# Kernel optimization log

Hardware: AMD Instinct MI355X
Metric: run time of the kernel (lower is better)

The kernel has to match this reference:

```python
import jax, jax.numpy as jnp
import numpy as np

B, L, C, DK, M, R = 8, 2048, 512, 64, 8, 64
H = 2 * C  # GLU hidden size
NEG = -32767.0  # -2**15 + 1 masked_fill value


def _ln(x, g, b):
    m = x.mean(-1, keepdims=True)
    v = jnp.mean((x - m) ** 2, axis=-1, keepdims=True)
    return (x - m) * jax.lax.rsqrt(v + 1e-5) * g + b


def setup_inputs() -> dict:
    key = jax.random.key(0)
    ks = jax.random.split(key, 16)
    p = lambda k, sh: 0.02 * jax.random.normal(k, sh, dtype=jnp.float32)
    return {
        "qx": jax.random.normal(ks[0], (B, L, C), dtype=jnp.float32),
        "vx": jax.random.normal(ks[1], (B, L, C), dtype=jnp.float32),
        "maskPAD2": jax.random.randint(ks[2], (B, 1, L), 0, 2),
        "WQ1": p(ks[3], (C, M * DK)), "WK1": p(ks[4], (C, M * DK)),
        "WV1": p(ks[5], (C, M * DK)), "WO1": p(ks[6], (M * DK, C)),
        "qln_g": jnp.ones((C,), jnp.float32), "qln_b": jnp.zeros((C,), jnp.float32),
        "Wp": p(ks[7], (C, R)), "bp": jnp.zeros((R,), jnp.float32),
        "Wq2": p(ks[8], (C, DK)), "bq2": jnp.zeros((DK,), jnp.float32),
        "Wk2": p(ks[9], (C, DK)), "bk2": jnp.zeros((DK,), jnp.float32),
        "Wv2": p(ks[10], (C, H)), "bv2": jnp.zeros((H,), jnp.float32),
        "Wu": p(ks[11], (C, H)), "bu": jnp.zeros((H,), jnp.float32),
        "Wo2": p(ks[12], (H, C)), "bo2": jnp.zeros((C,), jnp.float32),
        "ln_g": jnp.ones((C,), jnp.float32), "ln_b": jnp.zeros((C,), jnp.float32),
    }


def _forward(qx, vx, maskPAD2, WQ1, WK1, WV1, WO1, qln_g, qln_b,
             Wp, bp, Wq2, bq2, Wk2, bk2, Wv2, bv2, Wu, bu, Wo2, bo2, ln_g, ln_b):
    b, ql, c = qx.shape
    # ---- SelfAttention_CumNext(qx, qx, qx) ----
    div = jnp.arange(1, ql + 1, dtype=qx.dtype)[None, :, None]
    vc = jnp.cumsum(qx, axis=1) / div                      # running mean, [B,L,C]
    q = (qx @ WQ1).reshape(b, ql, M, DK).transpose(0, 2, 1, 3)   # [B,M,L,dk]
    k = (vc @ WK1).reshape(b, ql, M, DK).transpose(0, 2, 1, 3)
    v = (vc @ WV1).reshape(b, ql, M, DK).transpose(0, 2, 1, 3)
    scores1 = jnp.sum(q[:, :, 1:] * k[:, :, :-1], axis=-1, keepdims=True) / np.sqrt(DK)
    z = jax.nn.sigmoid(scores1) * v[:, :, :-1]             # [B,M,L-1,dk]
    z = z.transpose(0, 2, 1, 3).reshape(b, ql - 1, M * DK) @ WO1
    z = jnp.pad(z, ((0, 0), (1, 0), (0, 0)))               # shift right by 1
    qx = _ln(qx + z, qln_g, qln_b)
    # ---- GLU gate ----
    gate = jax.nn.silu(qx @ Wu + bu)                       # [B,L,2C]
    # ---- Linformer-style pseudo attention over vx ----
    pScore = vx @ Wp + bp                                  # [B,kvL,r]
    mask = (maskPAD2[:, 0] == 0)[..., None]                # [B,kvL,1]
    pScore = jnp.where(mask, NEG, pScore)
    pAlpha = jax.nn.softmax(pScore, axis=1)                # softmax over kvL
    pkvx = jnp.einsum('blr,blc->brc', pAlpha, vx)          # [B,r,C]
    queries = jax.nn.silu(qx @ Wq2 + bq2)                  # [B,L,dk]
    keys = jax.nn.silu(pkvx @ Wk2 + bk2)                   # [B,r,dk]
    values = jax.nn.silu(pkvx @ Wv2 + bv2)                 # [B,r,2C]
    scores2 = jnp.einsum('bld,brd->blr', queries, keys) / np.sqrt(DK)
    alpha = jax.nn.softmax(scores2, axis=-1)
    z2 = jnp.einsum('blr,brh->blh', alpha, values)         # [B,L,2C]
    z2 = (gate * z2) @ Wo2 + bo2                           # [B,L,C]
    return _ln(qx + z2, ln_g, ln_b)


def reference(qx, vx, maskPAD2, WQ1, WK1, WV1, WO1, qln_g, qln_b,
              Wp, bp, Wq2, bq2, Wk2, bk2, Wv2, bv2, Wu, bu, Wo2, bo2, ln_g, ln_b):
    return _forward(qx, vx, maskPAD2, WQ1, WK1, WV1, WO1, qln_g, qln_b,
                    Wp, bp, Wq2, bq2, Wk2, bk2, Wv2, bv2, Wu, bu, Wo2, bo2, ln_g, ln_b)
```

## Files before the change

kernel.cpp:

```cpp
#include <hip/hip_runtime.h>
#include <hip/hip_bf16.h>

#define B_ 8
#define L_ 2048
#define C_ 512
#define DK_ 64
#define M_ 8
#define R_ 64
#define H_ 1024
#define N_ (B_*L_)
#define NEG_ (-32767.0f)
#define NSEG 32
#define SEGLEN 64

typedef short bf16x8 __attribute__((ext_vector_type(8)));
typedef unsigned short us8 __attribute__((ext_vector_type(8)));
typedef float f32x4v __attribute__((ext_vector_type(4)));

__device__ __forceinline__ float siluf_(float x) { return x / (1.0f + expf(-x)); }

__device__ __forceinline__ unsigned short f2bf(float f) {
    __hip_bfloat16 h = __float2bfloat16(f);
    return __builtin_bit_cast(unsigned short, h);
}
__device__ __forceinline__ float bf2f(unsigned short u) {
    unsigned v = (unsigned)u << 16;
    return __builtin_bit_cast(float, v);
}

__device__ __forceinline__ void gload_lds16(const void* g, void* l) {
    __builtin_amdgcn_global_load_lds(
        (const __attribute__((address_space(1))) unsigned int*)(uintptr_t)g,
        (__attribute__((address_space(3))) unsigned int*)(unsigned)(uintptr_t)l,
        16, 0, 0);
}

__global__ __launch_bounds__(256) void cvt2_kernel(const float* __restrict__ s0,
                                                   const float* __restrict__ s1,
                                                   unsigned short* __restrict__ d0,
                                                   unsigned short* __restrict__ d1) {
    const float* s = blockIdx.z ? s1 : s0;
    unsigned short* d = blockIdx.z ? d1 : d0;
    const size_t i = ((size_t)blockIdx.x * 256 + threadIdx.x) * 8;
    const float4 v0 = *(const float4*)(s + i);
    const float4 v1 = *(const float4*)(s + i + 4);
    us8 o;
    o[0] = f2bf(v0.x); o[1] = f2bf(v0.y); o[2] = f2bf(v0.z); o[3] = f2bf(v0.w);
    o[4] = f2bf(v1.x); o[5] = f2bf(v1.y); o[6] = f2bf(v1.z); o[7] = f2bf(v1.w);
    *(us8*)(d + i) = o;
}

struct WtDesc { const float* src; unsigned short* dst; int K; int N; };
struct WtArgs { WtDesc d[10]; };

__global__ __launch_bounds__(256) void wtrans_all_kernel(WtArgs a) {
    const WtDesc w = a.d[blockIdx.z];
    const int n0 = blockIdx.x * 32, k0 = blockIdx.y * 32;
    if (n0 >= w.N || k0 >= w.K) return;
    __shared__ float t[32][33];
    const int tx = threadIdx.x, ty = threadIdx.y;
    #pragma unroll
    for (int i = 0; i < 32; i += 8)
        t[ty + i][tx] = w.src[(size_t)(k0 + ty + i) * w.N + n0 + tx];
    __syncthreads();
    #pragma unroll
    for (int i = 0; i < 32; i += 8)
        w.dst[(size_t)(n0 + ty + i) * w.K + k0 + tx] = f2bf(t[tx][ty + i]);
}

__global__ __launch_bounds__(512) void seg_sum_kernel(const unsigned short* __restrict__ qx,
                                                      float* __restrict__ segsum) {
    const int seg = blockIdx.x, b = blockIdx.y, c = threadIdx.x;
    const unsigned short* p = qx + ((size_t)b * L_ + (size_t)seg * SEGLEN) * C_ + c;
    float s = 0.f;
    #pragma unroll 8
    for (int i = 0; i < SEGLEN; ++i) s += bf2f(p[(size_t)i * C_]);
    segsum[((size_t)b * NSEG + seg) * C_ + c] = s;
}

__global__ __launch_bounds__(512) void seg_scan_kernel(const unsigned short* __restrict__ qx,
                                                       const float* __restrict__ segsum,
                                                       unsigned short* __restrict__ vc) {
    const int seg = blockIdx.x, b = blockIdx.y, c = threadIdx.x;
    float off = 0.f;
    for (int s = 0; s < seg; ++s) off += segsum[((size_t)b * NSEG + s) * C_ + c];
    const unsigned short* p = qx + ((size_t)b * L_ + (size_t)seg * SEGLEN) * C_ + c;
    unsigned short* o = vc + ((size_t)b * L_ + (size_t)seg * SEGLEN) * C_ + c;
    float run = off;
    for (int i = 0; i < SEGLEN; ++i) {
        run += bf2f(p[(size_t)i * C_]);
        const int l = seg * SEGLEN + i;
        o[(size_t)i * C_] = f2bf(run / (float)(l + 1));
    }
}

template<int BN, int ACT, bool BIAS, int OUT>
__global__ __launch_bounds__(256) void gemm_bf16(const unsigned short* __restrict__ A,
                                                 const unsigned short* __restrict__ Wt,
                                                 const float* __restrict__ bias,
                                                 void* __restrict__ Cout,
                                                 int K, int N) {
    constexpr int BK = 64;
    constexpr int WN = BN / 2;
    constexpr int TN = WN / 16;
    __shared__ unsigned short Alds[128 * BK];
    __shared__ unsigned short Blds[BN * BK];
    const int tid = threadIdx.x;
    const int w = tid >> 6, lane = tid & 63;
    const int wm = w >> 1, wn = w & 1;
    const int m0 = blockIdx.x * 128, n0 = blockIdx.y * BN;

    f32x4v acc[4][TN];
    #pragma unroll
    for (int m = 0; m < 4; ++m)
        #pragma unroll
        for (int n = 0; n < TN; ++n)
            acc[m][n] = f32x4v{0.f, 0.f, 0.f, 0.f};

    const int lrow = lane >> 3;
    const int lk = (lane & 7) * 8;

    for (int k0 = 0; k0 < K; k0 += BK) {
        __syncthreads();
        #pragma unroll
        for (int i = 0; i < 4; ++i) {
            const int c = w * 4 + i;
            const int row = c * 8 + lrow;
            gload_lds16(A + (size_t)(m0 + row) * K + k0 + lk, (char*)Alds + c * 1024);
        }
        #pragma unroll
        for (int i = 0; i < BN / 32; ++i) {
            const int c = w * (BN / 32) + i;
            const int col = c * 8 + lrow;
            gload_lds16(Wt + (size_t)(n0 + col) * K + k0 + lk, (char*)Blds + c * 1024);
        }
        __syncthreads();
        #pragma unroll
        for (int kk = 0; kk < 2; ++kk) {
            const int ko = kk * 64 + (lane >> 4) * 16;
            bf16x8 af[4], bfr[TN];
            #pragma unroll
            for (int m = 0; m < 4; ++m)
                af[m] = *(const bf16x8*)((const char*)Alds + (wm * 64 + m * 16 + (lane & 15)) * 128 + ko);
            #pragma unroll
            for (int n = 0; n < TN; ++n)
                bfr[n] = *(const bf16x8*)((const char*)Blds + (wn * WN + n * 16 + (lane & 15)) * 128 + ko);
            #pragma unroll
            for (int m = 0; m < 4; ++m)
                #pragma unroll
                for (int n = 0; n < TN; ++n)
                    acc[m][n] = __builtin_amdgcn_mfma_f32_16x16x32_bf16(af[m], bfr[n], acc[m][n], 0, 0, 0);
        }
    }
    const int r0 = (lane >> 4) * 4;
    #pragma unroll
    for (int n = 0; n < TN; ++n) {
        const int gc = n0 + wn * WN + n * 16 + (lane & 15);
        float bv = 0.f;
        if constexpr (BIAS) bv = bias[gc];
        #pragma unroll
        for (int m = 0; m < 4; ++m) {
            const int gr = m0 + wm * 64 + m * 16 + r0;
            float val[4];
            #pragma unroll
            for (int r = 0; r < 4; ++r) {
                val[r] = acc[m][n][r] + bv;
                if constexpr (ACT == 1) val[r] = siluf_(val[r]);
            }
            if constexpr (OUT == 0) {
                #pragma unroll
                for (int r = 0; r < 4; ++r)
                    ((float*)Cout)[(size_t)(gr + r) * N + gc] = val[r];
            } else if constexpr (OUT == 1) {
                #pragma unroll
                for (int r = 0; r < 4; ++r)
                    ((unsigned short*)Cout)[(size_t)(gr + r) * N + gc] = f2bf(val[r]);
            } else {
                ushort4 pk;
                pk.x = f2bf(val[0]); pk.y = f2bf(val[1]);
                pk.z = f2bf(val[2]); pk.w = f2bf(val[3]);
                *(ushort4*)((unsigned short*)Cout + ((size_t)(gr >> 6) * N + gc) * 64 + (gr & 63)) = pk;
            }
        }
    }
}

__global__ __launch_bounds__(512) void attn1_kernel(const unsigned short* __restrict__ Q,
                                                    const unsigned short* __restrict__ KV,
                                                    unsigned short* __restrict__ zbf) {
    const int l = blockIdx.x, b = blockIdx.y;
    const size_t row = ((size_t)b * L_ + l) * 512;
    if (l == 0) { zbf[row + threadIdx.x] = 0; return; }
    const size_t rowp = ((size_t)b * L_ + l - 1) * 1024;
    const float qv = bf2f(Q[row + threadIdx.x]);
    const float kv = bf2f(KV[rowp + threadIdx.x]);
    float p = qv * kv;
    #pragma unroll
    for (int o = 32; o; o >>= 1) p += __shfl_xor(p, o);
    const float s = p * 0.125f;
    const float sig = 1.0f / (1.0f + expf(-s));
    const float vv = bf2f(KV[rowp + 512 + threadIdx.x]);
    zbf[row + threadIdx.x] = f2bf(sig * vv);
}

__global__ __launch_bounds__(256) void ln_kernel(const float* __restrict__ X,
                                                 const float* __restrict__ Y,
                                                 const float* __restrict__ g,
                                                 const float* __restrict__ beta,
                                                 float* __restrict__ out,
                                                 unsigned short* __restrict__ outb) {
    const int w = threadIdx.x >> 6, lane = threadIdx.x & 63;
    const size_t row = (size_t)blockIdx.x * 4 + w;
    const float4* x4 = (const float4*)(X + row * C_);
    const float4* y4 = (const float4*)(Y + row * C_);
    float v[8];
    const float4 a = x4[lane * 2 + 0], b2 = x4[lane * 2 + 1];
    const float4 c = y4[lane * 2 + 0], d = y4[lane * 2 + 1];
    v[0] = a.x + c.x; v[1] = a.y + c.y; v[2] = a.z + c.z; v[3] = a.w + c.w;
    v[4] = b2.x + d.x; v[5] = b2.y + d.y; v[6] = b2.z + d.z; v[7] = b2.w + d.w;
    float s = 0.f;
    #pragma unroll
    for (int j = 0; j < 8; ++j) s += v[j];
    #pragma unroll
    for (int o = 32; o; o >>= 1) s += __shfl_xor(s, o);
    const float mean = s * (1.0f / 512.0f);
    float q = 0.f;
    #pragma unroll
    for (int j = 0; j < 8; ++j) { const float t = v[j] - mean; q += t * t; }
    #pragma unroll
    for (int o = 32; o; o >>= 1) q += __shfl_xor(q, o);
    const float rstd = rsqrtf(q * (1.0f / 512.0f) + 1e-5f);
    const float4 g0 = ((const float4*)g)[lane * 2], g1 = ((const float4*)g)[lane * 2 + 1];
    const float4 bb0 = ((const float4*)beta)[lane * 2], bb1 = ((const float4*)beta)[lane * 2 + 1];
    float o8[8];
    o8[0] = (v[0] - mean) * rstd * g0.x + bb0.x;
    o8[1] = (v[1] - mean) * rstd * g0.y + bb0.y;
    o8[2] = (v[2] - mean) * rstd * g0.z + bb0.z;
    o8[3] = (v[3] - mean) * rstd * g0.w + bb0.w;
    o8[4] = (v[4] - mean) * rstd * g1.x + bb1.x;
    o8[5] = (v[5] - mean) * rstd * g1.y + bb1.y;
    o8[6] = (v[6] - mean) * rstd * g1.z + bb1.z;
    o8[7] = (v[7] - mean) * rstd * g1.w + bb1.w;
    float4 o0, o1;
    o0.x = o8[0]; o0.y = o8[1]; o0.z = o8[2]; o0.w = o8[3];
    o1.x = o8[4]; o1.y = o8[5]; o1.z = o8[6]; o1.w = o8[7];
    ((float4*)(out + row * C_))[lane * 2 + 0] = o0;
    ((float4*)(out + row * C_))[lane * 2 + 1] = o1;
    if (outb) {
        us8 pk;
        #pragma unroll
        for (int j = 0; j < 8; ++j) pk[j] = f2bf(o8[j]);
        *(us8*)(outb + row * C_ + lane * 8) = pk;
    }
}

__global__ __launch_bounds__(256) void psoftmax_kernel(const float* __restrict__ pscore,
                                                       const int* __restrict__ mask,
                                                       float* __restrict__ pAlpha) {
    const int r = blockIdx.x, b = blockIdx.y, t = threadIdx.x;
    __shared__ float red[256];
    float sv[8];
    float lm = -3.4e38f;
    #pragma unroll
    for (int i = 0; i < 8; ++i) {
        const int l = t + i * 256;
        float x = pscore[((size_t)b * L_ + l) * R_ + r];
        if (mask[(size_t)b * L_ + l] == 0) x = NEG_;
        sv[i] = x; lm = fmaxf(lm, x);
    }
    red[t] = lm; __syncthreads();
    for (int o = 128; o; o >>= 1) { if (t < o) red[t] = fmaxf(red[t], red[t + o]); __syncthreads(); }
    const float mx = red[0]; __syncthreads();
    float ls = 0.f;
    #pragma unroll
    for (int i = 0; i < 8; ++i) { sv[i] = expf(sv[i] - mx); ls += sv[i]; }
    red[t] = ls; __syncthreads();
    for (int o = 128; o; o >>= 1) { if (t < o) red[t] += red[t + o]; __syncthreads(); }
    const float inv = 1.0f / red[0];
    #pragma unroll
    for (int i = 0; i < 8; ++i)
        pAlpha[((size_t)b * L_ + t + i * 256) * R_ + r] = sv[i] * inv;
}

__global__ __launch_bounds__(256) void pkv_partial_kernel(const float* __restrict__ pAlpha,
                                                          const float* __restrict__ vx,
                                                          float* __restrict__ part) {
    const int ct = blockIdx.x, ks = blockIdx.y, b = blockIdx.z;
    constexpr int KT = 16;
    __shared__ float Pa[KT][64 + 4];
    __shared__ float Vx[KT][64 + 4];
    const int tid = threadIdx.x;
    const int trow = tid >> 4, tcol = tid & 15;
    float acc[4][4];
    #pragma unroll
    for (int i = 0; i < 4; ++i)
        #pragma unroll
        for (int j = 0; j < 4; ++j) acc[i][j] = 0.f;
    const int l0 = ks * 256;
    for (int kk = 0; kk < 256; kk += KT) {
        const int lrow = tid >> 4;
        const int q4 = (tid & 15) << 2;
        const size_t lidx = (size_t)b * L_ + l0 + kk + lrow;
        *(float4*)&Pa[lrow][q4] = *(const float4*)(pAlpha + lidx * R_ + q4);
        *(float4*)&Vx[lrow][q4] = *(const float4*)(vx + lidx * C_ + ct * 64 + q4);
        __syncthreads();
        #pragma unroll
        for (int k = 0; k < KT; ++k) {
            float a[4], v[4];
            *(float4*)&a[0] = *(const float4*)&Pa[k][trow * 4];
            *(float4*)&v[0] = *(const float4*)&Vx[k][tcol * 4];
            #pragma unroll
            for (int i = 0; i < 4; ++i)
                #pragma unroll
                for (int j = 0; j < 4; ++j)
                    acc[i][j] = fmaf(a[i], v[j], acc[i][j]);
        }
        __syncthreads();
    }
    #pragma unroll
    for (int i = 0; i < 4; ++i) {
        const int r = trow * 4 + i;
        float4 vv;
        vv.x = acc[i][0]; vv.y = acc[i][1]; vv.z = acc[i][2]; vv.w = acc[i][3];
        *(float4*)(part + (((size_t)b * 8 + ks) * R_ + r) * C_ + ct * 64 + tcol * 4) = vv;
    }
}

__global__ __launch_bounds__(256) void pkv_reduce_kernel(const float* __restrict__ part,
                                                         unsigned short* __restrict__ pkvx) {
    const size_t idx = (size_t)blockIdx.x * 256 + threadIdx.x;
    const size_t b = idx / ((size_t)R_ * C_);
    const size_t rem = idx % ((size_t)R_ * C_);
    float s = 0.f;
    #pragma unroll
    for (int ks = 0; ks < 8; ++ks) s += part[(b * 8 + ks) * ((size_t)R_ * C_) + rem];
    pkvx[idx] = f2bf(s);
}

__global__ __launch_bounds__(256) void attn2_kernel(const unsigned short* __restrict__ q,
                                                    const unsigned short* __restrict__ k,
                                                    const unsigned short* __restrict__ vT,
                                                    const unsigned short* __restrict__ gate,
                                                    unsigned short* __restrict__ hb) {
    const int b = blockIdx.y, l0 = blockIdx.x * 32;
    const int tid = threadIdx.x, w = tid >> 6, lane = tid & 63;
    __shared__ float sc_s[32][68];
    __shared__ unsigned short al_s[32][72];

    {
        f32x4v acc[2];
        acc[0] = f32x4v{0.f,0.f,0.f,0.f}; acc[1] = f32x4v{0.f,0.f,0.f,0.f};
        const int r0 = w * 16;
        #pragma unroll
        for (int kk = 0; kk < 2; ++kk) {
            const bf16x8 bfr = *(const bf16x8*)(k + ((size_t)b * 64 + r0 + (lane & 15)) * 64 + kk * 32 + (lane >> 4) * 8);
            #pragma unroll
            for (int m = 0; m < 2; ++m) {
                const bf16x8 af = *(const bf16x8*)(q + ((size_t)b * L_ + l0 + m * 16 + (lane & 15)) * 64 + kk * 32 + (lane >> 4) * 8);
                acc[m] = __builtin_amdgcn_mfma_f32_16x16x32_bf16(af, bfr, acc[m], 0, 0, 0);
            }
        }
        #pragma unroll
        for (int m = 0; m < 2; ++m)
            #pragma unroll
            for (int i = 0; i < 4; ++i)
                sc_s[m * 16 + (lane >> 4) * 4 + i][r0 + (lane & 15)] = acc[m][i];
    }
    __syncthreads();
    {
        const int t = tid >> 3, rg = tid & 7;
        float v[8];
        float mx = -3.4e38f;
        #pragma unroll
        for (int j = 0; j < 8; ++j) { v[j] = sc_s[t][rg * 8 + j] * 0.125f; mx = fmaxf(mx, v[j]); }
        #pragma unroll
        for (int o = 1; o < 8; o <<= 1) mx = fmaxf(mx, __shfl_xor(mx, o));
        float es = 0.f;
        #pragma unroll
        for (int j = 0; j < 8; ++j) { v[j] = expf(v[j] - mx); es += v[j]; }
        #pragma unroll
        for (int o = 1; o < 8; o <<= 1) es += __shfl_xor(es, o);
        const float inv = 1.0f / es;
        #pragma unroll
        for (int j = 0; j < 8; ++j) al_s[t][rg * 8 + j] = f2bf(v[j] * inv);
    }
    __syncthreads();
    bf16x8 bl[2][2];
    #pragma unroll
    for (int n = 0; n < 2; ++n)
        #pragma unroll
        for (int kk = 0; kk < 2; ++kk)
            bl[n][kk] = *(const bf16x8*)&al_s[n * 16 + (lane & 15)][kk * 32 + (lane >> 4) * 8];
    const int hbase = w * 256;
    #pragma unroll 4
    for (int mi = 0; mi < 16; ++mi) {
        const int h0 = hbase + mi * 16;
        const unsigned short* ap = vT + ((size_t)b * H_ + h0 + (lane & 15)) * 64 + (lane >> 4) * 8;
        const bf16x8 a0 = *(const bf16x8*)(ap);
        const bf16x8 a1 = *(const bf16x8*)(ap + 32);
        f32x4v acc[2];
        acc[0] = f32x4v{0.f,0.f,0.f,0.f}; acc[1] = f32x4v{0.f,0.f,0.f,0.f};
        #pragma unroll
        for (int n = 0; n < 2; ++n) {
            acc[n] = __builtin_amdgcn_mfma_f32_16x16x32_bf16(a0, bl[n][0], acc[n], 0, 0, 0);
            acc[n] = __builtin_amdgcn_mfma_f32_16x16x32_bf16(a1, bl[n][1], acc[n], 0, 0, 0);
        }
        #pragma unroll
        for (int n = 0; n < 2; ++n) {
            const size_t base = ((size_t)b * L_ + l0 + n * 16 + (lane & 15)) * H_ + h0 + (lane >> 4) * 4;
            const ushort4 g = *(const ushort4*)(gate + base);
            ushort4 o;
            o.x = f2bf(bf2f(g.x) * acc[n][0]);
            o.y = f2bf(bf2f(g.y) * acc[n][1]);
            o.z = f2bf(bf2f(g.z) * acc[n][2]);
            o.w = f2bf(bf2f(g.w) * acc[n][3]);
            *(ushort4*)(hb + base) = o;
        }
    }
}

extern "C" void kernel_launch(void* const* d_in, const int* in_sizes, int n_in,
                              void* d_out, int out_size, void* d_ws, size_t ws_size,
                              hipStream_t stream) {
    const float* qx   = (const float*)d_in[0];
    const float* vx   = (const float*)d_in[1];
    const int*   maskPAD2 = (const int*)d_in[2];
    const float* WQ1  = (const float*)d_in[3];
    const float* WK1  = (const float*)d_in[4];
    const float* WV1  = (const float*)d_in[5];
    const float* WO1  = (const float*)d_in[6];
    const float* qln_g = (const float*)d_in[7];
    const float* qln_b = (const float*)d_in[8];
    const float* Wp   = (const float*)d_in[9];
    const float* bp   = (const float*)d_in[10];
    const float* Wq2  = (const float*)d_in[11];
    const float* bq2  = (const float*)d_in[12];
    const float* Wk2  = (const float*)d_in[13];
    const float* bk2  = (const float*)d_in[14];
    const float* Wv2  = (const float*)d_in[15];
    const float* bv2  = (const float*)d_in[16];
    const float* Wu   = (const float*)d_in[17];
    const float* bu   = (const float*)d_in[18];
    const float* Wo2  = (const float*)d_in[19];
    const float* bo2  = (const float*)d_in[20];
    const float* ln_g = (const float*)d_in[21];
    const float* ln_b = (const float*)d_in[22];
    float* out = (float*)d_out;

    char* p = (char*)d_ws;
    const size_t NC2 = (size_t)N_ * C_ * 2;
    unsigned short* qx_bf = (unsigned short*)p; p += NC2;
    unsigned short* Q_bf  = (unsigned short*)p; p += NC2;
    unsigned short* KV_bf = (unsigned short*)p; p += 2 * NC2;
    unsigned short* vc_bf = (unsigned short*)p; p += NC2;
    float* t1    = (float*)p; p += (size_t)N_ * C_ * 4;
    float* qx1f  = (float*)p; p += (size_t)N_ * C_ * 4;
    unsigned short* vx_bf = (unsigned short*)p; p += NC2;
    float* pscore  = (float*)p; p += (size_t)N_ * R_ * 4;
    float* pAlpha  = (float*)p; p += (size_t)N_ * R_ * 4;
    unsigned short* queries = (unsigned short*)p; p += (size_t)N_ * DK_ * 2;
    unsigned short* keysB   = (unsigned short*)p; p += (size_t)B_ * R_ * DK_ * 2;
    unsigned short* valT    = (unsigned short*)p; p += (size_t)B_ * H_ * R_ * 2;
    unsigned short* pkvx_bf = (unsigned short*)p; p += (size_t)B_ * R_ * C_ * 2;
    float* part    = (float*)p; p += (size_t)B_ * 8 * R_ * C_ * 4;
    float* segsum  = (float*)p; p += (size_t)B_ * NSEG * C_ * 4;
    unsigned short* wq1t  = (unsigned short*)p; p += (size_t)512 * C_ * 2;
    unsigned short* wkv1t = (unsigned short*)p; p += (size_t)1024 * C_ * 2;
    unsigned short* wo1t  = (unsigned short*)p; p += (size_t)C_ * 512 * 2;
    unsigned short* wpt   = (unsigned short*)p; p += (size_t)R_ * C_ * 2;
    unsigned short* wq2t  = (unsigned short*)p; p += (size_t)DK_ * C_ * 2;
    unsigned short* wk2t  = (unsigned short*)p; p += (size_t)DK_ * C_ * 2;
    unsigned short* wv2t  = (unsigned short*)p; p += (size_t)H_ * C_ * 2;
    unsigned short* wut   = (unsigned short*)p; p += (size_t)H_ * C_ * 2;
    unsigned short* wo2t  = (unsigned short*)p; p += (size_t)C_ * H_ * 2;

    unsigned short* zin_bf = qx_bf;
    unsigned short* h_bf   = qx_bf;
    unsigned short* gate   = KV_bf;
    unsigned short* qx1_bf = vc_bf;
    float* t2 = t1;

    cvt2_kernel<<<dim3((N_ * C_) / (256 * 8), 1, 2), 256, 0, stream>>>(qx, vx, qx_bf, vx_bf);
    WtArgs wa;
    wa.d[0] = {WQ1, wq1t, 512, 512};
    wa.d[1] = {WK1, wkv1t, 512, 512};
    wa.d[2] = {WV1, wkv1t + (size_t)512 * 512, 512, 512};
    wa.d[3] = {WO1, wo1t, 512, 512};
    wa.d[4] = {Wp,  wpt,  512, 64};
    wa.d[5] = {Wq2, wq2t, 512, 64};
    wa.d[6] = {Wk2, wk2t, 512, 64};
    wa.d[7] = {Wv2, wv2t, 512, 1024};
    wa.d[8] = {Wu,  wut,  512, 1024};
    wa.d[9] = {Wo2, wo2t, 1024, 512};
    wtrans_all_kernel<<<dim3(32, 32, 10), dim3(32, 8), 0, stream>>>(wa);
    seg_sum_kernel<<<dim3(NSEG, B_), 512, 0, stream>>>(qx_bf, segsum);
    seg_scan_kernel<<<dim3(NSEG, B_), 512, 0, stream>>>(qx_bf, segsum, vc_bf);
    gemm_bf16<128, 0, false, 1><<<dim3(N_/128, 4), 256, 0, stream>>>(qx_bf, wq1t, nullptr, Q_bf, 512, 512);
    gemm_bf16<128, 0, false, 1><<<dim3(N_/128, 8), 256, 0, stream>>>(vc_bf, wkv1t, nullptr, KV_bf, 512, 1024);
    attn1_kernel<<<dim3(L_, B_), 512, 0, stream>>>(Q_bf, KV_bf, zin_bf);
    gemm_bf16<128, 0, false, 0><<<dim3(N_/128, 4), 256, 0, stream>>>(zin_bf, wo1t, nullptr, t1, 512, 512);
    ln_kernel<<<N_/4, 256, 0, stream>>>(qx, t1, qln_g, qln_b, qx1f, qx1_bf);
    gemm_bf16<128, 1, true, 1><<<dim3(N_/128, 8), 256, 0, stream>>>(qx1_bf, wut, bu, gate, 512, 1024);
    gemm_bf16<64, 0, true, 0><<<dim3(N_/128, 1), 256, 0, stream>>>(vx_bf, wpt, bp, pscore, 512, 64);
    psoftmax_kernel<<<dim3(R_, B_), 256, 0, stream>>>(pscore, maskPAD2, pAlpha);
    pkv_partial_kernel<<<dim3(8, 8, B_), 256, 0, stream>>>(pAlpha, vx, part);
    pkv_reduce_kernel<<<(B_ * R_ * C_) / 256, 256, 0, stream>>>(part, pkvx_bf);
    gemm_bf16<64, 1, true, 1><<<dim3(N_/128, 1), 256, 0, stream>>>(qx1_bf, wq2t, bq2, queries, 512, 64);
    gemm_bf16<64, 1, true, 1><<<dim3((B_*R_)/128, 1), 256, 0, stream>>>(pkvx_bf, wk2t, bk2, keysB, 512, 64);
    gemm_bf16<128, 1, true, 2><<<dim3((B_*R_)/128, 8), 256, 0, stream>>>(pkvx_bf, wv2t, bv2, valT, 512, 1024);
    attn2_kernel<<<dim3(L_/32, B_), 256, 0, stream>>>(queries, keysB, valT, gate, h_bf);
    gemm_bf16<128, 0, true, 0><<<dim3(N_/128, 4), 256, 0, stream>>>(h_bf, wo2t, bo2, t2, 1024, 512);
    ln_kernel<<<N_/4, 256, 0, stream>>>(qx1f, t2, ln_g, ln_b, out, nullptr);
}
```

Baseline: 496.8 us.

## Stage GEMM epilogues through LDS, merge small GEMM launches, vectorize attn1

```diff
diff --git a/kernel.cpp b/kernel.cpp
--- a/kernel.cpp
+++ b/kernel.cpp
@@ -95,112 +95,216 @@
 }
 
 template<int BN, int ACT, bool BIAS, int OUT>
+__device__ __forceinline__ void gemm_body(char* smem,
+        const unsigned short* __restrict__ A, const unsigned short* __restrict__ Wt,
+        const float* __restrict__ bias, void* __restrict__ Cout,
+        int K, int N, int m0, int n0, int tid) {
+    constexpr int BK = 64;
+    constexpr int WN = BN / 2;
+    constexpr int TN = WN / 16;
+    unsigned short* Alds = (unsigned short*)smem;
+    unsigned short* Blds = (unsigned short*)(smem + 16384);
+    const int w = tid >> 6, lane = tid & 63;
+    const int wm = w >> 1, wn = w & 1;
+
+    f32x4v acc[4][TN];
+    #pragma unroll
+    for (int m = 0; m < 4; ++m)
+        #pragma unroll
+        for (int n = 0; n < TN; ++n)
+            acc[m][n] = f32x4v{0.f, 0.f, 0.f, 0.f};
+
+    const int lrow = lane >> 3;
+    const int lk = (lane & 7) * 8;
+
+    for (int k0 = 0; k0 < K; k0 += BK) {
+        __syncthreads();
+        #pragma unroll
+        for (int i = 0; i < 4; ++i) {
+            const int c = w * 4 + i;
+            const int row = c * 8 + lrow;
+            gload_lds16(A + (size_t)(m0 + row) * K + k0 + lk, (char*)Alds + c * 1024);
+        }
+        #pragma unroll
+        for (int i = 0; i < BN / 32; ++i) {
+            const int c = w * (BN / 32) + i;
+            const int col = c * 8 + lrow;
+            gload_lds16(Wt + (size_t)(n0 + col) * K + k0 + lk, (char*)Blds + c * 1024);
+        }
+        __syncthreads();
+        #pragma unroll
+        for (int kk = 0; kk < 2; ++kk) {
+            const int ko = kk * 64 + (lane >> 4) * 16;
+            bf16x8 af[4], bfr[TN];
+            #pragma unroll
+            for (int m = 0; m < 4; ++m)
+                af[m] = *(const bf16x8*)((const char*)Alds + (wm * 64 + m * 16 + (lane & 15)) * 128 + ko);
+            #pragma unroll
+            for (int n = 0; n < TN; ++n)
+                bfr[n] = *(const bf16x8*)((const char*)Blds + (wn * WN + n * 16 + (lane & 15)) * 128 + ko);
+            #pragma unroll
+            for (int m = 0; m < 4; ++m)
+                #pragma unroll
+                for (int n = 0; n < TN; ++n)
+                    acc[m][n] = __builtin_amdgcn_mfma_f32_16x16x32_bf16(af[m], bfr[n], acc[m][n], 0, 0, 0);
+        }
+    }
+
+    const int r0 = (lane >> 4) * 4;
+    float bv[TN];
+    #pragma unroll
+    for (int n = 0; n < TN; ++n)
+        bv[n] = BIAS ? bias[n0 + wn * WN + n * 16 + (lane & 15)] : 0.f;
+
+    if constexpr (OUT == 1) {
+        __syncthreads();
+        unsigned short* stg = (unsigned short*)smem;
+        #pragma unroll
+        for (int n = 0; n < TN; ++n) {
+            const int cl = wn * WN + n * 16 + (lane & 15);
+            #pragma unroll
+            for (int m = 0; m < 4; ++m)
+                #pragma unroll
+                for (int r = 0; r < 4; ++r) {
+                    float val = acc[m][n][r] + bv[n];
+                    if constexpr (ACT == 1) val = siluf_(val);
+                    stg[(wm * 64 + m * 16 + r0 + r) * BN + cl] = f2bf(val);
+                }
+        }
+        __syncthreads();
+        constexpr int CH = 128 * BN / 8 / 256;
+        #pragma unroll
+        for (int i = 0; i < CH; ++i) {
+            const int idx = i * 256 + tid;
+            const int row = (idx * 8) / BN, col = (idx * 8) % BN;
+            *(us8*)((unsigned short*)Cout + (size_t)(m0 + row) * N + n0 + col) = *(const us8*)&stg[idx * 8];
+        }
+    } else if constexpr (OUT == 2) {
+        __syncthreads();
+        unsigned short* stg = (unsigned short*)smem;
+        #pragma unroll
+        for (int n = 0; n < TN; ++n) {
+            const int cl = wn * WN + n * 16 + (lane & 15);
+            #pragma unroll
+            for (int m = 0; m < 4; ++m)
+                #pragma unroll
+                for (int r = 0; r < 4; ++r) {
+                    float val = acc[m][n][r] + bv[n];
+                    if constexpr (ACT == 1) val = siluf_(val);
+                    stg[(wm * BN + cl) * 72 + m * 16 + r0 + r] = f2bf(val);
+                }
+        }
+        __syncthreads();
+        constexpr int CH = 2 * BN * 64 / 8 / 256;
+        #pragma unroll
+        for (int i = 0; i < CH; ++i) {
+            const int idx = i * 256 + tid;
+            const int vrow = idx >> 3, j = (idx & 7) * 8;
+            const int h = vrow >= BN ? 1 : 0;
+            const int col = vrow & (BN - 1);
+            *(us8*)((unsigned short*)Cout + (((size_t)(m0 >> 6) + h) * N + n0 + col) * 64 + j)
+                = *(const us8*)&stg[vrow * 72 + j];
+        }
+    } else {
+        float* stgf = (float*)smem;
+        #pragma unroll
+        for (int pass = 0; pass < 2; ++pass) {
+            __syncthreads();
+            if (wm == pass) {
+                #pragma unroll
+                for (int n = 0; n < TN; ++n) {
+                    const int cl = wn * WN + n * 16 + (lane & 15);
+                    #pragma unroll
+                    for (int m = 0; m < 4; ++m)
+                        #pragma unroll
+                        for (int r = 0; r < 4; ++r) {
+                            float val = acc[m][n][r] + bv[n];
+                            if constexpr (ACT == 1) val = siluf_(val);
+                            stgf[(m * 16 + r0 + r) * BN + cl] = val;
+                        }
+                }
+            }
+            __syncthreads();
+            constexpr int CH = 64 * BN / 4 / 256;
+            #pragma unroll
+            for (int i = 0; i < CH; ++i) {
+                const int idx = i * 256 + tid;
+                const int row = (idx * 4) / BN, col = (idx * 4) % BN;
+                *(float4*)((float*)Cout + (size_t)(m0 + pass * 64 + row) * N + n0 + col)
+                    = *(const float4*)&stgf[idx * 4];
+            }
+        }
+    }
+}
+
+template<int BN, int ACT, bool BIAS, int OUT>
 __global__ __launch_bounds__(256) void gemm_bf16(const unsigned short* __restrict__ A,
                                                  const unsigned short* __restrict__ Wt,
                                                  const float* __restrict__ bias,
                                                  void* __restrict__ Cout,
                                                  int K, int N) {
-    constexpr int BK = 64;
-    constexpr int WN = BN / 2;
-    constexpr int TN = WN / 16;
-    __shared__ unsigned short Alds[128 * BK];
-    __shared__ unsigned short Blds[BN * BK];
-    const int tid = threadIdx.x;
-    const int w = tid >> 6, lane = tid & 63;
-    const int wm = w >> 1, wn = w & 1;
-    const int m0 = blockIdx.x * 128, n0 = blockIdx.y * BN;
-
-    f32x4v acc[4][TN];
-    #pragma unroll
-    for (int m = 0; m < 4; ++m)
-        #pragma unroll
-        for (int n = 0; n < TN; ++n)
-            acc[m][n] = f32x4v{0.f, 0.f, 0.f, 0.f};
-
-    const int lrow = lane >> 3;
-    const int lk = (lane & 7) * 8;
-
-    for (int k0 = 0; k0 < K; k0 += BK) {
-        __syncthreads();
-        #pragma unroll
-        for (int i = 0; i < 4; ++i) {
-            const int c = w * 4 + i;
-            const int row = c * 8 + lrow;
-            gload_lds16(A + (size_t)(m0 + row) * K + k0 + lk, (char*)Alds + c * 1024);
-        }
-        #pragma unroll
-        for (int i = 0; i < BN / 32; ++i) {
-            const int c = w * (BN / 32) + i;
-            const int col = c * 8 + lrow;
-            gload_lds16(Wt + (size_t)(n0 + col) * K + k0 + lk, (char*)Blds + c * 1024);
-        }
-        __syncthreads();
-        #pragma unroll
-        for (int kk = 0; kk < 2; ++kk) {
-            const int ko = kk * 64 + (lane >> 4) * 16;
-            bf16x8 af[4], bfr[TN];
-            #pragma unroll
-            for (int m = 0; m < 4; ++m)
-                af[m] = *(const bf16x8*)((const char*)Alds + (wm * 64 + m * 16 + (lane & 15)) * 128 + ko);
-            #pragma unroll
-            for (int n = 0; n < TN; ++n)
-                bfr[n] = *(const bf16x8*)((const char*)Blds + (wn * WN + n * 16 + (lane & 15)) * 128 + ko);
-            #pragma unroll
-            for (int m = 0; m < 4; ++m)
-                #pragma unroll
-                for (int n = 0; n < TN; ++n)
-                    acc[m][n] = __builtin_amdgcn_mfma_f32_16x16x32_bf16(af[m], bfr[n], acc[m][n], 0, 0, 0);
-        }
-    }
-    const int r0 = (lane >> 4) * 4;
-    #pragma unroll
-    for (int n = 0; n < TN; ++n) {
-        const int gc = n0 + wn * WN + n * 16 + (lane & 15);
-        float bv = 0.f;
-        if constexpr (BIAS) bv = bias[gc];
-        #pragma unroll
-        for (int m = 0; m < 4; ++m) {
-            const int gr = m0 + wm * 64 + m * 16 + r0;
-            float val[4];
-            #pragma unroll
-            for (int r = 0; r < 4; ++r) {
-                val[r] = acc[m][n][r] + bv;
-                if constexpr (ACT == 1) val[r] = siluf_(val[r]);
-            }
-            if constexpr (OUT == 0) {
-                #pragma unroll
-                for (int r = 0; r < 4; ++r)
-                    ((float*)Cout)[(size_t)(gr + r) * N + gc] = val[r];
-            } else if constexpr (OUT == 1) {
-                #pragma unroll
-                for (int r = 0; r < 4; ++r)
-                    ((unsigned short*)Cout)[(size_t)(gr + r) * N + gc] = f2bf(val[r]);
-            } else {
-                ushort4 pk;
-                pk.x = f2bf(val[0]); pk.y = f2bf(val[1]);
-                pk.z = f2bf(val[2]); pk.w = f2bf(val[3]);
-                *(ushort4*)((unsigned short*)Cout + ((size_t)(gr >> 6) * N + gc) * 64 + (gr & 63)) = pk;
-            }
-        }
-    }
-}
-
-__global__ __launch_bounds__(512) void attn1_kernel(const unsigned short* __restrict__ Q,
+    __shared__ char smem[BN == 128 ? 32768 : 24576];
+    gemm_body<BN, ACT, BIAS, OUT>(smem, A, Wt, bias, Cout, K, N,
+                                  blockIdx.x * 128, blockIdx.y * BN, threadIdx.x);
+}
+
+__global__ __launch_bounds__(256) void gemm_qkv(const unsigned short* __restrict__ qxA,
+                                                const unsigned short* __restrict__ wq,
+                                                unsigned short* __restrict__ Qo,
+                                                const unsigned short* __restrict__ vcA,
+                                                const unsigned short* __restrict__ wkv,
+                                                unsigned short* __restrict__ KVo) {
+    __shared__ char smem[32768];
+    if (blockIdx.y < 4)
+        gemm_body<128, 0, false, 1>(smem, qxA, wq, nullptr, Qo, 512, 512,
+                                    blockIdx.x * 128, blockIdx.y * 128, threadIdx.x);
+    else
+        gemm_body<128, 0, false, 1>(smem, vcA, wkv, nullptr, KVo, 512, 1024,
+                                    blockIdx.x * 128, (blockIdx.y - 4) * 128, threadIdx.x);
+}
+
+__global__ __launch_bounds__(256) void gemm_kv2(const unsigned short* __restrict__ pkvx,
+                                                const unsigned short* __restrict__ wk2,
+                                                const float* __restrict__ bk2,
+                                                unsigned short* __restrict__ keys,
+                                                const unsigned short* __restrict__ wv2,
+                                                const float* __restrict__ bv2,
+                                                unsigned short* __restrict__ valT) {
+    __shared__ char smem[24576];
+    if (blockIdx.y == 0)
+        gemm_body<64, 1, true, 1>(smem, pkvx, wk2, bk2, keys, 512, 64,
+                                  blockIdx.x * 128, 0, threadIdx.x);
+    else
+        gemm_body<64, 1, true, 2>(smem, pkvx, wv2, bv2, valT, 512, 1024,
+                                  blockIdx.x * 128, (blockIdx.y - 1) * 64, threadIdx.x);
+}
+
+__global__ __launch_bounds__(256) void attn1_kernel(const unsigned short* __restrict__ Q,
                                                     const unsigned short* __restrict__ KV,
                                                     unsigned short* __restrict__ zbf) {
-    const int l = blockIdx.x, b = blockIdx.y;
-    const size_t row = ((size_t)b * L_ + l) * 512;
-    if (l == 0) { zbf[row + threadIdx.x] = 0; return; }
-    const size_t rowp = ((size_t)b * L_ + l - 1) * 1024;
-    const float qv = bf2f(Q[row + threadIdx.x]);
-    const float kv = bf2f(KV[rowp + threadIdx.x]);
-    float p = qv * kv;
-    #pragma unroll
-    for (int o = 32; o; o >>= 1) p += __shfl_xor(p, o);
-    const float s = p * 0.125f;
-    const float sig = 1.0f / (1.0f + expf(-s));
-    const float vv = bf2f(KV[rowp + 512 + threadIdx.x]);
-    zbf[row + threadIdx.x] = f2bf(sig * vv);
+    const int w = threadIdx.x >> 6, lane = threadIdx.x & 63;
+    const size_t row = (size_t)blockIdx.x * 4 + w;
+    const int l = (int)(row & (L_ - 1));
+    unsigned short* zr = zbf + row * 512 + lane * 8;
+    if (l == 0) {
+        us8 z;
+        #pragma unroll
+        for (int j = 0; j < 8; ++j) z[j] = 0;
+        *(us8*)zr = z;
+        return;
+    }
+    const us8 q8 = *(const us8*)(Q + row * 512 + lane * 8);
+    const us8 k8 = *(const us8*)(KV + (row - 1) * 1024 + lane * 8);
+    float p = 0.f;
+    #pragma unroll
+    for (int j = 0; j < 8; ++j) p += bf2f(q8[j]) * bf2f(k8[j]);
+    p += __shfl_xor(p, 1); p += __shfl_xor(p, 2); p += __shfl_xor(p, 4);
+    const float sig = 1.0f / (1.0f + expf(-p * 0.125f));
+    const us8 v8 = *(const us8*)(KV + (row - 1) * 1024 + 512 + lane * 8);
+    us8 o;
+    #pragma unroll
+    for (int j = 0; j < 8; ++j) o[j] = f2bf(sig * bf2f(v8[j]));
+    *(us8*)zr = o;
 }
 
 __global__ __launch_bounds__(256) void ln_kernel(const float* __restrict__ X,
@@ -495,20 +599,18 @@
     wtrans_all_kernel<<<dim3(32, 32, 10), dim3(32, 8), 0, stream>>>(wa);
     seg_sum_kernel<<<dim3(NSEG, B_), 512, 0, stream>>>(qx_bf, segsum);
     seg_scan_kernel<<<dim3(NSEG, B_), 512, 0, stream>>>(qx_bf, segsum, vc_bf);
-    gemm_bf16<128, 0, false, 1><<<dim3(N_/128, 4), 256, 0, stream>>>(qx_bf, wq1t, nullptr, Q_bf, 512, 512);
-    gemm_bf16<128, 0, false, 1><<<dim3(N_/128, 8), 256, 0, stream>>>(vc_bf, wkv1t, nullptr, KV_bf, 512, 1024);
-    attn1_kernel<<<dim3(L_, B_), 512, 0, stream>>>(Q_bf, KV_bf, zin_bf);
-    gemm_bf16<128, 0, false, 0><<<dim3(N_/128, 4), 256, 0, stream>>>(zin_bf, wo1t, nullptr, t1, 512, 512);
-    ln_kernel<<<N_/4, 256, 0, stream>>>(qx, t1, qln_g, qln_b, qx1f, qx1_bf);
-    gemm_bf16<128, 1, true, 1><<<dim3(N_/128, 8), 256, 0, stream>>>(qx1_bf, wut, bu, gate, 512, 1024);
-    gemm_bf16<64, 0, true, 0><<<dim3(N_/128, 1), 256, 0, stream>>>(vx_bf, wpt, bp, pscore, 512, 64);
+    gemm_qkv<<<dim3(N_ / 128, 12), 256, 0, stream>>>(qx_bf, wq1t, Q_bf, vc_bf, wkv1t, KV_bf);
+    attn1_kernel<<<N_ / 4, 256, 0, stream>>>(Q_bf, KV_bf, zin_bf);
+    gemm_bf16<128, 0, false, 0><<<dim3(N_ / 128, 4), 256, 0, stream>>>(zin_bf, wo1t, nullptr, t1, 512, 512);
+    ln_kernel<<<N_ / 4, 256, 0, stream>>>(qx, t1, qln_g, qln_b, qx1f, qx1_bf);
+    gemm_bf16<128, 1, true, 1><<<dim3(N_ / 128, 8), 256, 0, stream>>>(qx1_bf, wut, bu, gate, 512, 1024);
+    gemm_bf16<64, 0, true, 0><<<dim3(N_ / 128, 1), 256, 0, stream>>>(vx_bf, wpt, bp, pscore, 512, 64);
     psoftmax_kernel<<<dim3(R_, B_), 256, 0, stream>>>(pscore, maskPAD2, pAlpha);
     pkv_partial_kernel<<<dim3(8, 8, B_), 256, 0, stream>>>(pAlpha, vx, part);
     pkv_reduce_kernel<<<(B_ * R_ * C_) / 256, 256, 0, stream>>>(part, pkvx_bf);
-    gemm_bf16<64, 1, true, 1><<<dim3(N_/128, 1), 256, 0, stream>>>(qx1_bf, wq2t, bq2, queries, 512, 64);
-    gemm_bf16<64, 1, true, 1><<<dim3((B_*R_)/128, 1), 256, 0, stream>>>(pkvx_bf, wk2t, bk2, keysB, 512, 64);
-    gemm_bf16<128, 1, true, 2><<<dim3((B_*R_)/128, 8), 256, 0, stream>>>(pkvx_bf, wv2t, bv2, valT, 512, 1024);
-    attn2_kernel<<<dim3(L_/32, B_), 256, 0, stream>>>(queries, keysB, valT, gate, h_bf);
-    gemm_bf16<128, 0, true, 0><<<dim3(N_/128, 4), 256, 0, stream>>>(h_bf, wo2t, bo2, t2, 1024, 512);
-    ln_kernel<<<N_/4, 256, 0, stream>>>(qx1f, t2, ln_g, ln_b, out, nullptr);
-}
+    gemm_bf16<64, 1, true, 1><<<dim3(N_ / 128, 1), 256, 0, stream>>>(qx1_bf, wq2t, bq2, queries, 512, 64);
+    gemm_kv2<<<dim3((B_ * R_) / 128, 17), 256, 0, stream>>>(pkvx_bf, wk2t, bk2, keysB, wv2t, bv2, valT);
+    attn2_kernel<<<dim3(L_ / 32, B_), 256, 0, stream>>>(queries, keysB, valT, gate, h_bf);
+    gemm_bf16<128, 0, true, 0><<<dim3(N_ / 128, 4), 256, 0, stream>>>(h_bf, wo2t, bo2, t2, 1024, 512);
+    ln_kernel<<<N_ / 4, 256, 0, stream>>>(qx1f, t2, ln_g, ln_b, out, nullptr);
+}
```

Result: faster. 455.2 us (-8.4%).
